# Kernel optimization log

Hardware: AMD Instinct MI355X
Metric: run time of the kernel (lower is better)

## Reference

```python
import jax, jax.numpy as jnp
import numpy as np
import math

B, N, D_MODEL = 2, 2048, 512
H, D_HEAD = 8, 64
D_FF = 2048
LN_EPS = 1e-5


def layer_norm(x, g, b):
    mu = jnp.mean(x, axis=-1, keepdims=True)
    var = jnp.mean(jnp.square(x - mu), axis=-1, keepdims=True)
    return (x - mu) * jax.lax.rsqrt(var + LN_EPS) * g + b


def setup_inputs() -> dict:
    key = jax.random.key(0)
    ks = jax.random.split(key, 12)
    s = lambda fan_in: 1.0 / math.sqrt(fan_in)
    inp = {
        "x": jax.random.normal(ks[0], (B, N, D_MODEL), dtype=jnp.float32),
        "mask": jax.random.randint(ks[1], (B, 1, N, N), 0, 2) > 0,
        # attention_pre: Linear(d_model -> 3*H*D_HEAD)
        "W_qkv": jax.random.uniform(ks[2], (D_MODEL, 3 * H * D_HEAD), minval=-s(D_MODEL), maxval=s(D_MODEL)),
        "b_qkv": jnp.zeros((3 * H * D_HEAD,), jnp.float32),
        # project: Linear(H*D_HEAD -> d_model)
        "W_proj": jax.random.uniform(ks[3], (H * D_HEAD, D_MODEL), minval=-s(H * D_HEAD), maxval=s(H * D_HEAD)),
        "b_proj": jnp.zeros((D_MODEL,), jnp.float32),
        "ln1_g": jnp.ones((D_MODEL,), jnp.float32),
        "ln1_b": jnp.zeros((D_MODEL,), jnp.float32),
        # mlp: fc(512->2048, relu), fc(2048->512, relu)  (activation on every layer)
        "W1": jax.random.uniform(ks[4], (D_MODEL, D_FF), minval=-s(D_MODEL), maxval=s(D_MODEL)),
        "b1": jnp.zeros((D_FF,), jnp.float32),
        "W2": jax.random.uniform(ks[5], (D_FF, D_MODEL), minval=-s(D_FF), maxval=s(D_FF)),
        "b2": jnp.zeros((D_MODEL,), jnp.float32),
        "ln2_g": jnp.ones((D_MODEL,), jnp.float32),
        "ln2_b": jnp.zeros((D_MODEL,), jnp.float32),
    }
    return inp


def reference(x, mask, W_qkv, b_qkv, W_proj, b_proj, ln1_g, ln1_b, W1, b1, W2, b2, ln2_g, ln2_b):
    # --- Attention (manual QKV matmul-softmax-matmul) ---
    qkv = x @ W_qkv + b_qkv                      # [B,N,3*H*Dh]
    q, k, v = jnp.split(qkv, 3, axis=2)          # each [B,N,H*Dh]
    def split_heads(t):
        return t.reshape(B, N, H, D_HEAD).transpose(0, 2, 1, 3)  # [B,H,N,Dh]
    q, k, v = split_heads(q), split_heads(k), split_heads(v)
    score = jnp.einsum('bhnd,bhmd->bhnm', q, k) / math.sqrt(D_HEAD)  # [B,H,N,N]
    score = jnp.where(mask, score, -1e9)
    score = jax.nn.softmax(score, axis=-1)
    attn = jnp.einsum('bhnm,bhmd->bhnd', score, v)   # [B,H,N,Dh]
    attn = attn.transpose(0, 2, 1, 3).reshape(B, N, H * D_HEAD)
    a = attn @ W_proj + b_proj                   # [B,N,D_MODEL]
    # --- residual + LN1 ---
    x = layer_norm(x + a, ln1_g, ln1_b)
    # --- MLP (relu after both layers, dropout p=0 = identity) ---
    m = jax.nn.relu(jax.nn.relu(x @ W1 + b1) @ W2 + b2)
    x = layer_norm(x + m, ln2_g, ln2_b)
    return x
```

## Files before the change

kernel.cpp:

```cpp
#include <hip/hip_runtime.h>
#include <math.h>

constexpr int BATCH  = 2;
constexpr int SEQ    = 2048;
constexpr int DMODEL = 512;
constexpr int NH     = 8;
constexpr int DHEAD  = 64;
constexpr int ROWS   = BATCH * SEQ;
constexpr size_t SZ  = (size_t)ROWS * DMODEL;
constexpr int NSPLIT = 4;

typedef __attribute__((ext_vector_type(8))) short bf16x8;
typedef __attribute__((ext_vector_type(4))) float f32x4;

__device__ __forceinline__ ushort f2bf(float f) {
    unsigned u = __float_as_uint(f);
    unsigned r = (u + 0x7FFFu + ((u >> 16) & 1u)) >> 16;
    return (ushort)r;
}
__device__ __forceinline__ float bf2f(ushort u) {
    return __uint_as_float((unsigned)u << 16);
}

__device__ __forceinline__ unsigned cvtpk_bf16(float lo, float hi) {
    unsigned r;
    asm("v_cvt_pk_bf16_f32 %0, %1, %2" : "=v"(r) : "v"(lo), "v"(hi));
    return r;
}

__device__ __forceinline__ void gload_lds16(const void* g, void* l) {
    __builtin_amdgcn_global_load_lds(
        (const __attribute__((address_space(1))) void*)g,
        (__attribute__((address_space(3))) void*)l, 16, 0, 0);
}

__global__ __launch_bounds__(256) void detect_mask_k(
    const uint4* __restrict__ m, int* __restrict__ flag)
{
    const int i = blockIdx.x * 256 + threadIdx.x;
    const uint4 v = m[i];
    unsigned b0 = 0, b1 = 0;
    #pragma unroll
    for (int c = 0; c < 4; ++c) {
        const unsigned u = (&v.x)[c];
        b0 |= (u > 1u) ? 1u : 0u;
        b1 |= (u != 0u && u != 0x3F800000u) ? 1u : 0u;
    }
    const int lane = threadIdx.x & 63;
    if (__any(b0) && lane == 0) atomicOr(flag, 1);
    if (__any(b1) && lane == 0) atomicOr(flag, 2);
}

__global__ __launch_bounds__(256) void prep_all_k(
    const float* __restrict__ x, ushort* __restrict__ xb,
    const float* __restrict__ Wq, const float* __restrict__ Wp,
    const float* __restrict__ W1w, const float* __restrict__ W2w,
    ushort* __restrict__ WqT, ushort* __restrict__ WpT,
    ushort* __restrict__ W1T, ushort* __restrict__ W2T,
    const void* __restrict__ maskp, const int* __restrict__ flagp,
    unsigned long long* __restrict__ bits)
{
    __shared__ ushort T[64][65];
    const int bid = blockIdx.x;
    const int t = threadIdx.x;

    if (bid < 2048) {
        const size_t i = ((size_t)bid * 256 + t) * 4;
        float4 v = *(const float4*)(x + i);
        ushort4 o;
        o.x = f2bf(v.x); o.y = f2bf(v.y); o.z = f2bf(v.z); o.w = f2bf(v.w);
        *(ushort4*)(xb + i) = o;
        return;
    }
    if (bid >= 2816) {
        const int w = (bid - 2816) * 4 + (t >> 6);
        const int lane = t & 63;
        const size_t idx = ((size_t)w << 6) + lane;
        const int f = *flagp;
        bool mv;
        if (!(f & 1))      mv = ((const int*)maskp)[idx] != 0;
        else if (!(f & 2)) mv = ((const float*)maskp)[idx] != 0.f;
        else               mv = ((const unsigned char*)maskp)[idx] != 0;
        unsigned long long bal = __ballot(mv);
        if (lane == 0) bits[w] = bal;
        return;
    }
    const int wb = bid - 2048;
    const float* W; ushort* Wt; int K, N, tix, tiy;
    if (wb < 192)      { W = Wq;  Wt = WqT; K = 512;  N = 1536; tix = wb % 24;        tiy = wb / 24; }
    else if (wb < 256) { W = Wp;  Wt = WpT; K = 512;  N = 512;  tix = (wb-192) % 8;   tiy = (wb-192) / 8; }
    else if (wb < 512) { W = W1w; Wt = W1T; K = 512;  N = 2048; tix = (wb-256) % 32;  tiy = (wb-256) / 32; }
    else               { W = W2w; Wt = W2T; K = 2048; N = 512;  tix = (wb-512) % 8;   tiy = (wb-512) / 8; }
    const int k0 = tiy * 64, n0 = tix * 64;
    const int r = t >> 4, c4 = (t & 15) * 4;
    #pragma unroll
    for (int it = 0; it < 4; ++it) {
        const int row = it*16 + r;
        float4 v = *(const float4*)&W[(size_t)(k0 + row) * N + n0 + c4];
        T[c4+0][row] = f2bf(v.x);
        T[c4+1][row] = f2bf(v.y);
        T[c4+2][row] = f2bf(v.z);
        T[c4+3][row] = f2bf(v.w);
    }
    __syncthreads();
    #pragma unroll
    for (int it = 0; it < 4; ++it) {
        const int row = it*16 + r;
        ushort4 o;
        o.x = T[row][c4+0]; o.y = T[row][c4+1];
        o.z = T[row][c4+2]; o.w = T[row][c4+3];
        *(ushort4*)&Wt[(size_t)(n0 + row) * K + k0 + c4] = o;
    }
}

template<int EPI, int BM, int BN>
__global__ __launch_bounds__(256) void mgemm_k(
    const ushort* __restrict__ A,
    const ushort* __restrict__ Wt,
    const float* __restrict__ bias,
    float* __restrict__ Cf, ushort* __restrict__ Cb,
    ushort* __restrict__ Qo, ushort* __restrict__ Ko, ushort* __restrict__ Vo,
    int M, int N, int K)
{
    constexpr int WM  = BM / 2, WN = BN / 2;
    constexpr int MF  = WM / 16, NF = WN / 16;
    constexpr int APW = BM / 32;
    constexpr int BPW = BN / 32;

    __shared__ ushort As[BM * 64];
    __shared__ ushort Bs[BN * 64];

    const int tid  = threadIdx.x;
    const int wid  = tid >> 6, lane = tid & 63;
    const int lq   = lane & 15, lg = lane >> 4;
    const int wr   = wid >> 1,  wc = wid & 1;
    const int bm   = blockIdx.y * BM, bn = blockIdx.x * BN;

    const int srow0 = lane >> 3;
    const int sch   = lane & 7;

    f32x4 acc[MF][NF] = {};

    for (int k0 = 0; k0 < K; k0 += 64) {
        __syncthreads();
        #pragma unroll
        for (int i = 0; i < APW; ++i) {
            const int seg = wid * APW + i;
            const int row = seg * 8 + srow0;
            const int c16 = sch ^ (row & 7);
            gload_lds16(A + (size_t)(bm + row) * K + k0 + c16 * 8, As + seg * 512);
        }
        #pragma unroll
        for (int i = 0; i < BPW; ++i) {
            const int seg = wid * BPW + i;
            const int row = seg * 8 + srow0;
            const int c16 = sch ^ (row & 7);
            gload_lds16(Wt + (size_t)(bn + row) * K + k0 + c16 * 8, Bs + seg * 512);
        }
        __syncthreads();

        #pragma unroll
        for (int ks = 0; ks < 2; ++ks) {
            bf16x8 af[MF], bfr[NF];
            #pragma unroll
            for (int m = 0; m < MF; ++m) {
                const int row = wr*WM + m*16 + lq;
                const int c16 = (ks*4 + lg) ^ (row & 7);
                af[m] = *(const bf16x8*)&As[row * 64 + c16 * 8];
            }
            #pragma unroll
            for (int n = 0; n < NF; ++n) {
                const int row = wc*WN + n*16 + lq;
                const int c16 = (ks*4 + lg) ^ (row & 7);
                bfr[n] = *(const bf16x8*)&Bs[row * 64 + c16 * 8];
            }
            #pragma unroll
            for (int m = 0; m < MF; ++m)
                #pragma unroll
                for (int n = 0; n < NF; ++n)
                    acc[m][n] = __builtin_amdgcn_mfma_f32_16x16x32_bf16(
                        af[m], bfr[n], acc[m][n], 0, 0, 0);
        }
    }

    #pragma unroll
    for (int m = 0; m < MF; ++m) {
        const int row0 = bm + wr*WM + m*16 + lg*4;
        #pragma unroll
        for (int n = 0; n < NF; ++n) {
            const int col = bn + wc*WN + n*16 + lq;
            const float bv = bias[col];
            float v[4];
            #pragma unroll
            for (int r = 0; r < 4; ++r) {
                v[r] = acc[m][n][r] + bv;
                if (EPI == 1 || EPI == 2) v[r] = fmaxf(v[r], 0.f);
            }
            if (EPI == 3) {
                const int part = col >> 9, hc = col & 511;
                const int hh = hc >> 6, d0 = hc & 63;
                const int bidx = row0 >> 11, nrow0 = row0 & 2047;
                if (part == 2) {
                    ushort4 pv;
                    pv.x = f2bf(v[0]); pv.y = f2bf(v[1]);
                    pv.z = f2bf(v[2]); pv.w = f2bf(v[3]);
                    *(ushort4*)(Vo + (((size_t)bidx*NH + hh)*DHEAD + d0)*SEQ + nrow0) = pv;
                } else {
                    ushort* dst = (part == 0) ? Qo : Ko;
                    #pragma unroll
                    for (int r = 0; r < 4; ++r)
                        dst[((((size_t)bidx*NH + hh)*SEQ + nrow0 + r) << 6) + d0] = f2bf(v[r]);
                }
            } else {
                #pragma unroll
                for (int r = 0; r < 4; ++r) {
                    const int row = row0 + r;
                    if (EPI == 1) Cb[(size_t)row * N + col] = f2bf(v[r]);
                    else          Cf[(size_t)row * N + col] = v[r];
                }
            }
        }
    }
}

__global__ __launch_bounds__(256, 4) void attn_mfma_k(
    const ushort* __restrict__ Qb, const ushort* __restrict__ Kb,
    const ushort* __restrict__ Vtb, const unsigned long long* __restrict__ mbits,
    ushort* __restrict__ Opart, float2* __restrict__ MLpart)
{
    __shared__ ushort Klds[2][64 * 64];
    __shared__ ushort Vlds[2][64 * 64];
    __shared__ ushort Plds[4][16 * 64];

    const int tid  = threadIdx.x;
    const int wid  = tid >> 6;
    const int lane = tid & 63;
    const int lq   = lane & 15;
    const int lg   = lane >> 4;

    const int tile = blockIdx.x & 31;
    const int bh   = blockIdx.x >> 5;
    const int b    = bh >> 3;
    const int qw   = tile * 64 + wid * 16;
    const int s    = blockIdx.y;
    const int c0   = s * 8, c1 = c0 + 8;

    const ushort* Qg = Qb + ((size_t)bh * SEQ + qw + lq) * DHEAD;
    const bf16x8 qf0 = *(const bf16x8*)(Qg + lg * 8);
    const bf16x8 qf1 = *(const bf16x8*)(Qg + 32 + lg * 8);

    const int srow0 = lane >> 3;
    const int sch   = lane & 7;
    const int gc8   = (sch ^ srow0) * 8;

    const ushort* kgb  = Kb  + (size_t)bh * SEQ * DHEAD
                             + (size_t)(wid*16 + srow0) * DHEAD + gc8;
    const ushort* vgb0 = Vtb + (size_t)bh * DHEAD * SEQ
                             + (size_t)(wid*16 + srow0) * SEQ + gc8;
    const ushort* vgb1 = vgb0 + 8 * SEQ;

    ushort* kd0 = &Klds[0][(wid*2)*512];
    ushort* kd1 = &Klds[1][(wid*2)*512];
    ushort* vd0 = &Vlds[0][(wid*2)*512];
    ushort* vd1 = &Vlds[1][(wid*2)*512];

    int kro[4][2], vro[4][2], pwo[4], pro[2];
    #pragma unroll
    for (int kt = 0; kt < 4; ++kt) {
        kro[kt][0] = ((kt*16 + lq)*64 + ((lg     ^ (lq&7))*8)) * 2;
        kro[kt][1] = ((kt*16 + lq)*64 + (((4+lg) ^ (lq&7))*8)) * 2;
        pwo[kt]    = (wid*1024 + lq*64 + (((kt*2 + (lg>>1)) ^ (lq&7))*8) + (lg&1)*4) * 2;
    }
    #pragma unroll
    for (int kk = 0; kk < 2; ++kk) {
        pro[kk] = (wid*1024 + lq*64 + (((kk*4+lg) ^ (lq&7))*8)) * 2;
        #pragma unroll
        for (int nt = 0; nt < 4; ++nt)
            vro[nt][kk] = ((nt*16 + lq)*64 + (((kk*4+lg) ^ (lq&7))*8)) * 2;
    }
    const char* kbase0 = (const char*)&Klds[0][0];
    const char* kbase1 = (const char*)&Klds[1][0];
    const char* vbase0 = (const char*)&Vlds[0][0];
    const char* vbase1 = (const char*)&Vlds[1][0];
    char*       pbase  = (char*)&Plds[0][0];

    const unsigned long long* mrow = mbits + ((size_t)b * SEQ + qw + lq) * (SEQ / 64);

    f32x4 o[4] = {};
    float mrun = -1e30f, lrun = 0.f;
    const float k2 = 0.125f * 1.44269504f;

    {
        const ushort* kp0  = kgb  + (size_t)c0 * 4096;
        const ushort* vq0  = vgb0 + c0 * 64;
        const ushort* vq1  = vgb1 + c0 * 64;
        gload_lds16(kp0,       kd0);
        gload_lds16(kp0 + 512, kd0 + 512);
        gload_lds16(vq0, vd0);
        gload_lds16(vq1, vd0 + 512);
    }
    const ushort* kp  = kgb  + (size_t)(c0 + 1) * 4096;
    const ushort* vp0 = vgb0 + (c0 + 1) * 64;
    const ushort* vp1 = vgb1 + (c0 + 1) * 64;
    __syncthreads();

#define ATTN_CHUNK(CC, KD, VD, KBASE, VBASE)                                   \
    {                                                                          \
        if ((CC) + 1 < c1) {                                                   \
            gload_lds16(kp,       (KD));                                       \
            gload_lds16(kp + 512, (KD) + 512);                                 \
            gload_lds16(vp0, (VD));                                            \
            gload_lds16(vp1, (VD) + 512);                                      \
            kp += 4096; vp0 += 64; vp1 += 64;                                  \
        }                                                                      \
        f32x4 st[4];                                                           \
        __builtin_amdgcn_s_setprio(1);                                         \
        _Pragma("unroll")                                                      \
        for (int kt = 0; kt < 4; ++kt) {                                       \
            bf16x8 kf0 = *(const bf16x8*)((KBASE) + kro[kt][0]);               \
            bf16x8 kf1 = *(const bf16x8*)((KBASE) + kro[kt][1]);               \
            f32x4 a = {};                                                      \
            a = __builtin_amdgcn_mfma_f32_16x16x32_bf16(kf0, qf0, a, 0, 0, 0); \
            a = __builtin_amdgcn_mfma_f32_16x16x32_bf16(kf1, qf1, a, 0, 0, 0); \
            st[kt] = a;                                                        \
        }                                                                      \
        __builtin_amdgcn_s_setprio(0);                                         \
        const unsigned long long mws = mrow[CC] >> (lg * 4);                   \
        const unsigned mlo = (unsigned)mws, mhi = (unsigned)(mws >> 32);       \
        float sv[16];                                                          \
        _Pragma("unroll")                                                      \
        for (int kt = 0; kt < 4; ++kt) {                                       \
            const unsigned half = (kt & 2) ? mhi : mlo;                        \
            _Pragma("unroll")                                                  \
            for (int r = 0; r < 4; ++r) {                                      \
                const unsigned bit = (half >> ((kt & 1)*16 + r)) & 1u;         \
                sv[kt*4 + r] = bit ? st[kt][r] * k2 : -1e9f;                   \
            }                                                                  \
        }                                                                      \
        float cmax = fmaxf(                                                    \
            fmaxf(fmaxf(fmaxf(sv[0],sv[1]),fmaxf(sv[2],sv[3])),                \
                  fmaxf(fmaxf(sv[4],sv[5]),fmaxf(sv[6],sv[7]))),               \
            fmaxf(fmaxf(fmaxf(sv[8],sv[9]),fmaxf(sv[10],sv[11])),              \
                  fmaxf(fmaxf(sv[12],sv[13]),fmaxf(sv[14],sv[15]))));          \
        cmax = fmaxf(cmax, __shfl_xor(cmax, 16));                              \
        cmax = fmaxf(cmax, __shfl_xor(cmax, 32));                              \
        float mnew = mrun, scale = 1.0f;                                       \
        if (!__all(cmax <= mrun)) {                                            \
            mnew  = fmaxf(mrun, cmax);                                         \
            scale = exp2f(mrun - mnew);                                        \
            float sc[4];                                                       \
            _Pragma("unroll")                                                  \
            for (int r = 0; r < 4; ++r) sc[r] = __shfl(scale, lg*4 + r);       \
            _Pragma("unroll")                                                  \
            for (int nt = 0; nt < 4; ++nt)                                     \
                _Pragma("unroll")                                              \
                for (int r = 0; r < 4; ++r) o[nt][r] *= sc[r];                 \
        }                                                                      \
        float ls[4];                                                           \
        _Pragma("unroll")                                                      \
        for (int kt = 0; kt < 4; ++kt) {                                       \
            const float p0 = exp2f(sv[kt*4+0] - mnew);                         \
            const float p1 = exp2f(sv[kt*4+1] - mnew);                         \
            const float p2 = exp2f(sv[kt*4+2] - mnew);                         \
            const float p3 = exp2f(sv[kt*4+3] - mnew);                         \
            ls[kt] = (p0 + p1) + (p2 + p3);                                    \
            uint2 pk;                                                          \
            pk.x = cvtpk_bf16(p0, p1);                                         \
            pk.y = cvtpk_bf16(p2, p3);                                         \
            *(uint2*)(pbase + pwo[kt]) = pk;                                   \
        }                                                                      \
        float lsum = (ls[0] + ls[1]) + (ls[2] + ls[3]);                        \
        lsum += __shfl_xor(lsum, 16);                                          \
        lsum += __shfl_xor(lsum, 32);                                          \
        lrun = lrun * scale + lsum;                                            \
        mrun = mnew;                                                           \
        __builtin_amdgcn_s_setprio(1);                                         \
        _Pragma("unroll")                                                      \
        for (int kk = 0; kk < 2; ++kk) {                                       \
            bf16x8 pf = *(const bf16x8*)(pbase + pro[kk]);                     \
            _Pragma("unroll")                                                  \
            for (int nt = 0; nt < 4; ++nt) {                                   \
                bf16x8 vf = *(const bf16x8*)((VBASE) + vro[nt][kk]);           \
                o[nt] = __builtin_amdgcn_mfma_f32_16x16x32_bf16(               \
                    pf, vf, o[nt], 0, 0, 0);                                   \
            }                                                                  \
        }                                                                      \
        __builtin_amdgcn_s_setprio(0);                                         \
        __syncthreads();                                                       \
    }

    for (int c = c0; c < c1; c += 2) {
        ATTN_CHUNK(c,     kd1, vd1, kbase0, vbase0);
        ATTN_CHUNK(c + 1, kd0, vd0, kbase1, vbase1);
    }
#undef ATTN_CHUNK

    #pragma unroll
    for (int nt = 0; nt < 4; ++nt)
        #pragma unroll
        for (int r = 0; r < 4; ++r) {
            const int qrow = qw + lg*4 + r;
            Opart[(((size_t)s*16 + bh)*SEQ + qrow)*64 + nt*16 + lq] = f2bf(o[nt][r]);
        }
    if (lg == 0) {
        float2 ml; ml.x = mrun; ml.y = lrun;
        MLpart[((size_t)s*16 + bh)*SEQ + qw + lq] = ml;
    }
}

__global__ __launch_bounds__(256) void attn_combine_k(
    const ushort* __restrict__ Op, const float2* __restrict__ ML,
    ushort* __restrict__ attnb)
{
    const int row  = blockIdx.x * 4 + (threadIdx.x >> 6);
    const int lane = threadIdx.x & 63;
    const int bh = row >> 11, q = row & 2047;
    const int b = bh >> 3, h = bh & 7;
    float2 ml[NSPLIT];
    float m = -1e30f;
    #pragma unroll
    for (int s = 0; s < NSPLIT; ++s) {
        ml[s] = ML[(size_t)s*16*SEQ + row];
        m = fmaxf(m, ml[s].x);
    }
    float l = 0.f, o = 0.f;
    #pragma unroll
    for (int s = 0; s < NSPLIT; ++s) {
        const float a = exp2f(ml[s].x - m);
        l += ml[s].y * a;
        o += bf2f(Op[((size_t)s*16*SEQ + row)*64 + lane]) * a;
    }
    attnb[((size_t)(b*SEQ + q))*DMODEL + h*DHEAD + lane] = f2bf(o / l);
}

__global__ __launch_bounds__(256) void add_ln_k(
    const float* __restrict__ X, const float* __restrict__ Aa,
    const float* __restrict__ gg, const float* __restrict__ bb,
    float* __restrict__ out, ushort* __restrict__ outb)
{
    const int r = blockIdx.x;
    const int t = threadIdx.x;
    const float2 x2 = ((const float2*)(X  + (size_t)r * DMODEL))[t];
    const float2 a2 = ((const float2*)(Aa + (size_t)r * DMODEL))[t];
    const float v0 = x2.x + a2.x, v1 = x2.y + a2.y;
    float s  = v0 + v1;
    float ss = v0*v0 + v1*v1;
    #pragma unroll
    for (int off = 32; off > 0; off >>= 1) {
        s  += __shfl_down(s,  off);
        ss += __shfl_down(ss, off);
    }
    __shared__ float ps[4], pss[4];
    const int wid = t >> 6;
    if ((t & 63) == 0) { ps[wid] = s; pss[wid] = ss; }
    __syncthreads();
    const float tot  = ps[0] + ps[1] + ps[2] + ps[3];
    const float tots = pss[0] + pss[1] + pss[2] + pss[3];
    const float mean = tot * (1.0f / DMODEL);
    const float var  = tots * (1.0f / DMODEL) - mean * mean;
    const float rstd = rsqrtf(var + 1e-5f);
    const float2 g2 = ((const float2*)gg)[t];
    const float2 b2 = ((const float2*)bb)[t];
    float2 r2;
    r2.x = (v0 - mean) * rstd * g2.x + b2.x;
    r2.y = (v1 - mean) * rstd * g2.y + b2.y;
    ((float2*)(out + (size_t)r * DMODEL))[t] = r2;
    if (outb) {
        ushort2 ob; ob.x = f2bf(r2.x); ob.y = f2bf(r2.y);
        *(ushort2*)(outb + (size_t)r * DMODEL + t*2) = ob;
    }
}

extern "C" void kernel_launch(void* const* d_in, const int* in_sizes, int n_in,
                              void* d_out, int out_size, void* d_ws, size_t ws_size,
                              hipStream_t stream)
{
    const float* x      = (const float*)d_in[0];
    const void*  mask   = d_in[1];
    const float* W_qkv  = (const float*)d_in[2];
    const float* b_qkv  = (const float*)d_in[3];
    const float* W_proj = (const float*)d_in[4];
    const float* b_proj = (const float*)d_in[5];
    const float* ln1_g  = (const float*)d_in[6];
    const float* ln1_b  = (const float*)d_in[7];
    const float* W1     = (const float*)d_in[8];
    const float* b1     = (const float*)d_in[9];
    const float* W2     = (const float*)d_in[10];
    const float* b2     = (const float*)d_in[11];
    const float* ln2_g  = (const float*)d_in[12];
    const float* ln2_b  = (const float*)d_in[13];

    float* ws = (float*)d_ws;
    ushort* xb    = (ushort*)ws;
    ushort* Qb    = (ushort*)(ws + SZ/2);
    ushort* Kb    = (ushort*)(ws + SZ);
    ushort* Vtb   = (ushort*)(ws + SZ + SZ/2);
    ushort* attnb = (ushort*)(ws + 2*SZ);
    ushort* Opart = (ushort*)(ws + 2*SZ + SZ/2);
    float2* MLp   = (float2*)(ws + 4*SZ + SZ/2);
    float*  ap    = ws + 2*SZ + SZ/2;
    float*  mbuf  = ws + 2*SZ;
    float*  x1    = ws + 3*SZ + SZ/2;
    ushort* x1b   = (ushort*)(ws + 4*SZ + SZ/2);
    ushort* hb    = (ushort*)ws;
    ushort* WqkvT = (ushort*)(ws + 5*SZ);
    ushort* WprojT= (ushort*)(ws + 5*SZ + 393216);
    ushort* W1T   = (ushort*)(ws + 5*SZ + 524288);
    ushort* W2T   = (ushort*)(ws + 5*SZ + 1048576);
    unsigned long long* bits = (unsigned long long*)(ws + 5*SZ + 1572864);
    int*    flag  = (int*)(ws + 5*SZ + 1572864 + 262144);

    float* out = (float*)d_out;

    hipMemsetAsync(flag, 0, 4, stream);
    detect_mask_k<<<64, 256, 0, stream>>>((const uint4*)mask, flag);
    prep_all_k<<<2816 + 32768, 256, 0, stream>>>(
        x, xb, W_qkv, W_proj, W1, W2, WqkvT, WprojT, W1T, W2T,
        mask, flag, bits);

    mgemm_k<3,64,128><<<dim3(12, 64), 256, 0, stream>>>(xb, WqkvT, b_qkv,
        nullptr, nullptr, Qb, Kb, Vtb, ROWS, 3*DMODEL, DMODEL);
    attn_mfma_k<<<dim3(BATCH*NH*(SEQ/64), NSPLIT), 256, 0, stream>>>(
        Qb, Kb, Vtb, bits, Opart, MLp);
    attn_combine_k<<<BATCH*NH*SEQ/4, 256, 0, stream>>>(Opart, MLp, attnb);
    mgemm_k<0,64,64><<<dim3(8, 64), 256, 0, stream>>>(attnb, WprojT, b_proj,
        ap, nullptr, nullptr, nullptr, nullptr, ROWS, DMODEL, DMODEL);
    add_ln_k<<<ROWS, 256, 0, stream>>>(x, ap, ln1_g, ln1_b, x1, x1b);
    mgemm_k<1,64,128><<<dim3(16, 64), 256, 0, stream>>>(x1b, W1T, b1,
        nullptr, hb, nullptr, nullptr, nullptr, ROWS, 2048, DMODEL);
    mgemm_k<2,64,64><<<dim3(8, 64), 256, 0, stream>>>(hb, W2T, b2,
        mbuf, nullptr, nullptr, nullptr, nullptr, ROWS, DMODEL, 2048);
    add_ln_k<<<ROWS, 256, 0, stream>>>(x1, mbuf, ln2_g, ln2_b, out, nullptr);
}
```

Baseline: 161.1 us.

## Store GEMM outputs and residuals in bf16, remap attention blocks, prefetch mask words

The projection and MLP GEMMs now write bf16 outputs instead of fp32. The LayerNorm kernels read bf16 inputs, and the second LayerNorm takes its residual from the bf16 copy of x1 rather than an fp32 copy. This cuts memory traffic in the epilogue and LayerNorm stages, at the cost of extra rounding error in the residual path. Separately, attention blocks are remapped so each XCD works on a contiguous pair of heads for better L2 locality, and the next chunk's mask word is loaded one iteration early.

New measurement: 158.4 us. Within noise of the previous version (-1.7%).

```diff
diff --git a/kernel.cpp b/kernel.cpp
--- a/kernel.cpp
+++ b/kernel.cpp
@@ -118,7 +118,7 @@
     const ushort* __restrict__ A,
     const ushort* __restrict__ Wt,
     const float* __restrict__ bias,
-    float* __restrict__ Cf, ushort* __restrict__ Cb,
+    ushort* __restrict__ Cb,
     ushort* __restrict__ Qo, ushort* __restrict__ Ko, ushort* __restrict__ Vo,
     int M, int N, int K)
 {
@@ -194,7 +194,7 @@
             #pragma unroll
             for (int r = 0; r < 4; ++r) {
                 v[r] = acc[m][n][r] + bv;
-                if (EPI == 1 || EPI == 2) v[r] = fmaxf(v[r], 0.f);
+                if (EPI == 1) v[r] = fmaxf(v[r], 0.f);
             }
             if (EPI == 3) {
                 const int part = col >> 9, hc = col & 511;
@@ -213,11 +213,8 @@
                 }
             } else {
                 #pragma unroll
-                for (int r = 0; r < 4; ++r) {
-                    const int row = row0 + r;
-                    if (EPI == 1) Cb[(size_t)row * N + col] = f2bf(v[r]);
-                    else          Cf[(size_t)row * N + col] = v[r];
-                }
+                for (int r = 0; r < 4; ++r)
+                    Cb[(size_t)(row0 + r) * N + col] = f2bf(v[r]);
             }
         }
     }
@@ -238,8 +235,11 @@
     const int lq   = lane & 15;
     const int lg   = lane >> 4;
 
-    const int tile = blockIdx.x & 31;
-    const int bh   = blockIdx.x >> 5;
+    const int raw  = blockIdx.x;
+    const int xcd  = raw & 7;
+    const int idx  = raw >> 3;
+    const int bh   = xcd * 2 + (idx >> 5);
+    const int tile = idx & 31;
     const int b    = bh >> 3;
     const int qw   = tile * 64 + wid * 16;
     const int s    = blockIdx.y;
@@ -302,11 +302,14 @@
     const ushort* kp  = kgb  + (size_t)(c0 + 1) * 4096;
     const ushort* vp0 = vgb0 + (c0 + 1) * 64;
     const ushort* vp1 = vgb1 + (c0 + 1) * 64;
+    unsigned long long mw_cur = mrow[c0];
     __syncthreads();
 
 #define ATTN_CHUNK(CC, KD, VD, KBASE, VBASE)                                   \
     {                                                                          \
+        unsigned long long mw_nxt = 0;                                         \
         if ((CC) + 1 < c1) {                                                   \
+            mw_nxt = mrow[(CC) + 1];                                           \
             gload_lds16(kp,       (KD));                                       \
             gload_lds16(kp + 512, (KD) + 512);                                 \
             gload_lds16(vp0, (VD));                                            \
@@ -325,7 +328,7 @@
             st[kt] = a;                                                        \
         }                                                                      \
         __builtin_amdgcn_s_setprio(0);                                         \
-        const unsigned long long mws = mrow[CC] >> (lg * 4);                   \
+        const unsigned long long mws = mw_cur >> (lg * 4);                     \
         const unsigned mlo = (unsigned)mws, mhi = (unsigned)(mws >> 32);       \
         float sv[16];                                                          \
         _Pragma("unroll")                                                      \
@@ -387,6 +390,7 @@
         }                                                                      \
         __builtin_amdgcn_s_setprio(0);                                         \
         __syncthreads();                                                       \
+        mw_cur = mw_nxt;                                                       \
     }
 
     for (int c = c0; c < c1; c += 2) {
@@ -433,16 +437,32 @@
     attnb[((size_t)(b*SEQ + q))*DMODEL + h*DHEAD + lane] = f2bf(o / l);
 }
 
+template<int XBF, int ABF>
 __global__ __launch_bounds__(256) void add_ln_k(
-    const float* __restrict__ X, const float* __restrict__ Aa,
+    const void* __restrict__ X, const void* __restrict__ Aa,
     const float* __restrict__ gg, const float* __restrict__ bb,
-    float* __restrict__ out, ushort* __restrict__ outb)
+    float* __restrict__ outf, ushort* __restrict__ outb)
 {
     const int r = blockIdx.x;
     const int t = threadIdx.x;
-    const float2 x2 = ((const float2*)(X  + (size_t)r * DMODEL))[t];
-    const float2 a2 = ((const float2*)(Aa + (size_t)r * DMODEL))[t];
-    const float v0 = x2.x + a2.x, v1 = x2.y + a2.y;
+    const size_t i2 = (size_t)r * 256 + t;
+    float x0, x1;
+    if (XBF) {
+        ushort2 u = ((const ushort2*)X)[i2];
+        x0 = bf2f(u.x); x1 = bf2f(u.y);
+    } else {
+        float2 f = ((const float2*)X)[i2];
+        x0 = f.x; x1 = f.y;
+    }
+    float a0, a1;
+    if (ABF) {
+        ushort2 u = ((const ushort2*)Aa)[i2];
+        a0 = bf2f(u.x); a1 = bf2f(u.y);
+    } else {
+        float2 f = ((const float2*)Aa)[i2];
+        a0 = f.x; a1 = f.y;
+    }
+    const float v0 = x0 + a0, v1 = x1 + a1;
     float s  = v0 + v1;
     float ss = v0*v0 + v1*v1;
     #pragma unroll
@@ -464,10 +484,10 @@
     float2 r2;
     r2.x = (v0 - mean) * rstd * g2.x + b2.x;
     r2.y = (v1 - mean) * rstd * g2.y + b2.y;
-    ((float2*)(out + (size_t)r * DMODEL))[t] = r2;
+    if (outf) ((float2*)outf)[i2] = r2;
     if (outb) {
         ushort2 ob; ob.x = f2bf(r2.x); ob.y = f2bf(r2.y);
-        *(ushort2*)(outb + (size_t)r * DMODEL + t*2) = ob;
+        ((ushort2*)outb)[i2] = ob;
     }
 }
 
@@ -498,10 +518,9 @@
     ushort* attnb = (ushort*)(ws + 2*SZ);
     ushort* Opart = (ushort*)(ws + 2*SZ + SZ/2);
     float2* MLp   = (float2*)(ws + 4*SZ + SZ/2);
-    float*  ap    = ws + 2*SZ + SZ/2;
-    float*  mbuf  = ws + 2*SZ;
-    float*  x1    = ws + 3*SZ + SZ/2;
-    ushort* x1b   = (ushort*)(ws + 4*SZ + SZ/2);
+    ushort* ap    = (ushort*)(ws + 2*SZ + SZ/2);
+    ushort* x1b   = (ushort*)(ws + 3*SZ);
+    ushort* mbuf  = (ushort*)(ws + 3*SZ + SZ/2);
     ushort* hb    = (ushort*)ws;
     ushort* WqkvT = (ushort*)(ws + 5*SZ);
     ushort* WprojT= (ushort*)(ws + 5*SZ + 393216);
@@ -519,16 +538,16 @@
         mask, flag, bits);
 
     mgemm_k<3,64,128><<<dim3(12, 64), 256, 0, stream>>>(xb, WqkvT, b_qkv,
-        nullptr, nullptr, Qb, Kb, Vtb, ROWS, 3*DMODEL, DMODEL);
+        nullptr, Qb, Kb, Vtb, ROWS, 3*DMODEL, DMODEL);
     attn_mfma_k<<<dim3(BATCH*NH*(SEQ/64), NSPLIT), 256, 0, stream>>>(
         Qb, Kb, Vtb, bits, Opart, MLp);
     attn_combine_k<<<BATCH*NH*SEQ/4, 256, 0, stream>>>(Opart, MLp, attnb);
-    mgemm_k<0,64,64><<<dim3(8, 64), 256, 0, stream>>>(attnb, WprojT, b_proj,
-        ap, nullptr, nullptr, nullptr, nullptr, ROWS, DMODEL, DMODEL);
-    add_ln_k<<<ROWS, 256, 0, stream>>>(x, ap, ln1_g, ln1_b, x1, x1b);
+    mgemm_k<4,64,64><<<dim3(8, 64), 256, 0, stream>>>(attnb, WprojT, b_proj,
+        ap, nullptr, nullptr, nullptr, ROWS, DMODEL, DMODEL);
+    add_ln_k<0,1><<<ROWS, 256, 0, stream>>>(x, ap, ln1_g, ln1_b, nullptr, x1b);
     mgemm_k<1,64,128><<<dim3(16, 64), 256, 0, stream>>>(x1b, W1T, b1,
-        nullptr, hb, nullptr, nullptr, nullptr, ROWS, 2048, DMODEL);
-    mgemm_k<2,64,64><<<dim3(8, 64), 256, 0, stream>>>(hb, W2T, b2,
-        mbuf, nullptr, nullptr, nullptr, nullptr, ROWS, DMODEL, 2048);
-    add_ln_k<<<ROWS, 256, 0, stream>>>(x1, mbuf, ln2_g, ln2_b, out, nullptr);
-}
+        hb, nullptr, nullptr, nullptr, ROWS, 2048, DMODEL);
+    mgemm_k<1,64,64><<<dim3(8, 64), 256, 0, stream>>>(hb, W2T, b2,
+        mbuf, nullptr, nullptr, nullptr, ROWS, DMODEL, 2048);
+    add_ln_k<1,1><<<ROWS, 256, 0, stream>>>(x1b, mbuf, ln2_g, ln2_b, out, nullptr);
+}
```
